# Kernel tuning notes

Hardware: AMD Instinct MI355X
Metric: run time of the kernel (lower is better)

## Reference

```python
import jax, jax.numpy as jnp
import numpy as np

N_NODES = 200000
N_EDGES = 6400000
IN_DIM = 15      # pfc_input_dim
POS_DIM = 4      # positional_dim
OUT_DIM = 2      # vtx_classes + 1


def setup_inputs() -> dict:
    key = jax.random.key(0)
    k1, k2, k3, k4, k5, k6, k7 = jax.random.split(key, 7)
    x_pfc = jax.random.normal(k1, (N_NODES, IN_DIM), dtype=jnp.float32)
    edge_index = jax.random.randint(k2, (2, N_EDGES), 0, N_NODES, dtype=jnp.int64)
    s_in = 1.0 / np.sqrt(IN_DIM)
    s_pos = 1.0 / np.sqrt(POS_DIM)
    # PointTransformerConv params: lin, lin_src, lin_dst (no bias), pos_nn = Linear(4, 2)
    W_lin = jax.random.uniform(k3, (OUT_DIM, IN_DIM), jnp.float32, -s_in, s_in)
    W_src = jax.random.uniform(k4, (OUT_DIM, IN_DIM), jnp.float32, -s_in, s_in)
    W_dst = jax.random.uniform(k5, (OUT_DIM, IN_DIM), jnp.float32, -s_in, s_in)
    W_pos = jax.random.uniform(k6, (OUT_DIM, POS_DIM), jnp.float32, -s_pos, s_pos)
    b_pos = jax.random.uniform(k7, (OUT_DIM,), jnp.float32, -s_pos, s_pos)
    return {"x_pfc": x_pfc, "edge_index": edge_index, "W_lin": W_lin,
            "W_src": W_src, "W_dst": W_dst, "W_pos": W_pos, "b_pos": b_pos}


def reference(x_pfc, edge_index, W_lin, W_src, W_dst, W_pos, b_pos):
    n = x_pfc.shape[0]
    pos = x_pfc[:, :POS_DIM]
    # original forward calls ptc_only(x, pos, edge_index.flip(0)):
    # source j = edge_index[1], target i = edge_index[0]
    j = edge_index[1]
    i = edge_index[0]
    # node-level linear maps (N x OUT_DIM)
    v = x_pfc @ W_lin.T
    a_src = x_pfc @ W_src.T
    a_dst = x_pfc @ W_dst.T
    # positional MLP on relative positions (E x OUT_DIM)
    delta = (pos[i] - pos[j]) @ W_pos.T + b_pos
    alpha = a_dst[i] - a_src[j] + delta
    # segment softmax over incoming edges of each target node i
    m = jax.ops.segment_max(alpha, i, num_segments=n)  # -inf for empty segments (never indexed)
    e = jnp.exp(alpha - m[i])
    denom = jax.ops.segment_sum(e, i, num_segments=n)
    attn = e / (denom[i] + 1e-16)
    msg = attn * (v[j] + delta)
    return jax.ops.segment_sum(msg, i, num_segments=n)
```

## Files before the change

### kernel.cpp

```cpp
#include <hip/hip_runtime.h>

#define N_NODES 200000
#define N_EDGES 6400000
#define IN_DIM 15
#define POS_DIM 4

#define CSHIFT 9
#define CMASK 511
#define CW 512
#define NCOARSE ((N_NODES + CW - 1) >> CSHIFT)
#define CHUNK 16384
#define NBLK ((N_EDGES + CHUNK - 1) / CHUNK)
#define CAP 17408
#define HCAP 8704

typedef unsigned uv4 __attribute__((ext_vector_type(4)));


__global__ void node_prep(const float* __restrict__ x,
                          const float* __restrict__ Wlin,
                          const float* __restrict__ Wsrc,
                          const float* __restrict__ Wpos,
                          float4* __restrict__ tabJ,
                          unsigned* __restrict__ gcnt)
{
    int n = blockIdx.x * blockDim.x + threadIdx.x;
    if (n < NCOARSE) gcnt[n] = 0u;
    if (n >= N_NODES) return;
    const float* xp = x + (long)n * IN_DIM;
    float xv[IN_DIM];
#pragma unroll
    for (int k = 0; k < IN_DIM; ++k) xv[k] = xp[k];

    float p0 = 0.f, p1 = 0.f;
#pragma unroll
    for (int k = 0; k < POS_DIM; ++k) {
        p0 += Wpos[k] * xv[k];
        p1 += Wpos[POS_DIM + k] * xv[k];
    }
    float v0 = 0.f, v1 = 0.f, as0 = 0.f, as1 = 0.f;
#pragma unroll
    for (int k = 0; k < IN_DIM; ++k) {
        float xk = xv[k];
        v0  += Wlin[k] * xk;  v1  += Wlin[IN_DIM + k] * xk;
        as0 += Wsrc[k] * xk;  as1 += Wsrc[IN_DIM + k] * xk;
    }
    tabJ[n] = make_float4(as0 + p0, as1 + p1, v0 - p0, v1 - p1);
}

__global__ void scatter_kernel(const int* __restrict__ idx,
                               unsigned* __restrict__ gcnt,
                               unsigned* __restrict__ packed)
{
    __shared__ unsigned stage[CHUNK];
    __shared__ unsigned cnt[512];
    __shared__ unsigned lloc[512];
    __shared__ unsigned gdst[NCOARSE];
    __shared__ unsigned wsum[8];
    int b = blockIdx.x;
    int t = threadIdx.x;
    int lane = t & 63, wid = t >> 6;
    long s0 = (long)b * CHUNK;
    int end = (int)min((long)CHUNK, (long)N_EDGES - s0);
    cnt[t] = 0u;
    __syncthreads();
    for (int e = t * 4; e < end; e += 2048) {
        int4 iv = *(const int4*)(idx + s0 + e);
        atomicAdd(&cnt[iv.x >> CSHIFT], 1u);
        atomicAdd(&cnt[iv.y >> CSHIFT], 1u);
        atomicAdd(&cnt[iv.z >> CSHIFT], 1u);
        atomicAdd(&cnt[iv.w >> CSHIFT], 1u);
    }
    __syncthreads();
    unsigned v = cnt[t];
    unsigned s = v;
#pragma unroll
    for (int off = 1; off < 64; off <<= 1) {
        unsigned u = __shfl_up(s, off, 64);
        if (lane >= off) s += u;
    }
    if (lane == 63) wsum[wid] = s;
    __syncthreads();
    unsigned woff = 0;
#pragma unroll
    for (int w = 0; w < 8; ++w) woff += (w < wid) ? wsum[w] : 0u;
    {
        unsigned ex = woff + s - v;
        lloc[t] = ex;
        cnt[t] = ex;
        if (t < NCOARSE) gdst[t] = atomicAdd(&gcnt[t], v);
    }
    __syncthreads();
    for (int e = t * 4; e < end; e += 2048) {
        int4 iv = *(const int4*)(idx + s0 + e);
        int4 jv = *(const int4*)(idx + N_EDGES + s0 + e);
        unsigned r0 = atomicAdd(&cnt[iv.x >> CSHIFT], 1u);
        unsigned r1 = atomicAdd(&cnt[iv.y >> CSHIFT], 1u);
        unsigned r2 = atomicAdd(&cnt[iv.z >> CSHIFT], 1u);
        unsigned r3 = atomicAdd(&cnt[iv.w >> CSHIFT], 1u);
        stage[r0] = ((unsigned)jv.x << CSHIFT) | (unsigned)(iv.x & CMASK);
        stage[r1] = ((unsigned)jv.y << CSHIFT) | (unsigned)(iv.y & CMASK);
        stage[r2] = ((unsigned)jv.z << CSHIFT) | (unsigned)(iv.z & CMASK);
        stage[r3] = ((unsigned)jv.w << CSHIFT) | (unsigned)(iv.w & CMASK);
    }
    __syncthreads();
    for (int bk = wid; bk < NCOARSE; bk += 8) {
        unsigned st  = lloc[bk];
        unsigned len = lloc[bk + 1] - st;
        unsigned gb  = gdst[bk];
        unsigned rem = (gb < (unsigned)CAP) ? (unsigned)CAP - gb : 0u;
        if (len > rem) len = rem;
        unsigned* dst = packed + (size_t)bk * CAP + gb;
        for (unsigned e = lane; e < len; e += 64u)
            dst[e] = stage[st + e];
    }
}

__global__ __launch_bounds__(256) void
bucket_agg_kernel(const unsigned* __restrict__ packed,
                  const unsigned* __restrict__ gcnt,
                  const float* __restrict__ x,
                  const float* __restrict__ Wdst,
                  const float* __restrict__ Wpos,
                  const float4* __restrict__ tabJ,
                  const float* __restrict__ bpos,
                  float2* __restrict__ out)
{
    __shared__ unsigned cache[HCAP + 512];
    __shared__ unsigned cnt[256], cur[256];
    __shared__ unsigned wsum[4];
    int blk = blockIdx.x;
    int k = blk >> 1;
    unsigned half = (unsigned)(blk & 1);
    int t = threadIdx.x;
    int lane = t & 63, wid = t >> 6;
    float b0 = bpos[0], b1 = bpos[1];
    int gn = (k << CSHIFT) + ((int)half << 8) + t;

    float p0 = 0.f, p1 = 0.f, ad0 = 0.f, ad1 = 0.f;
    if (gn < N_NODES) {
        const float* xp = x + (long)gn * IN_DIM;
        float xv[IN_DIM];
#pragma unroll
        for (int q = 0; q < IN_DIM; ++q) xv[q] = xp[q];
#pragma unroll
        for (int q = 0; q < POS_DIM; ++q) {
            p0 += Wpos[q] * xv[q];
            p1 += Wpos[POS_DIM + q] * xv[q];
        }
#pragma unroll
        for (int q = 0; q < IN_DIM; ++q) {
            ad0 += Wdst[q] * xv[q];
            ad1 += Wdst[IN_DIM + q] * xv[q];
        }
    }
    float a0 = ad0 + p0 + b0, a1 = ad1 + p1 + b1;
    float sn0 = 0.f, sn1 = 0.f, sd0 = 0.f, sd1 = 0.f;

    unsigned n = min(gcnt[k], (unsigned)CAP);
    const unsigned* pk = packed + (size_t)k * CAP;

#define KEEP(w) ((((w) & CMASK) >> 8) == half)
    cnt[t] = 0u;
    __syncthreads();
    for (unsigned e = 4u * t; e < n; e += 1024u) {
        uv4 p = *(const uv4*)(pk + e);
        if (KEEP(p.x))               atomicAdd(&cnt[p.x & 255u], 1u);
        if (e + 1 < n && KEEP(p.y))  atomicAdd(&cnt[p.y & 255u], 1u);
        if (e + 2 < n && KEEP(p.z))  atomicAdd(&cnt[p.z & 255u], 1u);
        if (e + 3 < n && KEEP(p.w))  atomicAdd(&cnt[p.w & 255u], 1u);
    }
    __syncthreads();
    unsigned v = cnt[t];
    unsigned s = v;
#pragma unroll
    for (int off = 1; off < 64; off <<= 1) {
        unsigned u = __shfl_up(s, off, 64);
        if (lane >= off) s += u;
    }
    if (lane == 63) wsum[wid] = s;
    __syncthreads();
    unsigned woff = 0;
#pragma unroll
    for (int w = 0; w < 4; ++w) woff += (w < wid) ? wsum[w] : 0u;
    unsigned deg = v;
    unsigned st  = woff + s - v + (unsigned)t;
    cur[t] = st;
    __syncthreads();
    for (unsigned e = 4u * t; e < n; e += 1024u) {
        uv4 p = __builtin_nontemporal_load((const uv4*)(pk + e));
        if (KEEP(p.x))              { unsigned pos = atomicAdd(&cur[p.x & 255u], 1u); cache[pos] = p.x >> CSHIFT; }
        if (e + 1 < n && KEEP(p.y)) { unsigned pos = atomicAdd(&cur[p.y & 255u], 1u); cache[pos] = p.y >> CSHIFT; }
        if (e + 2 < n && KEEP(p.z)) { unsigned pos = atomicAdd(&cur[p.z & 255u], 1u); cache[pos] = p.z >> CSHIFT; }
        if (e + 3 < n && KEEP(p.w)) { unsigned pos = atomicAdd(&cur[p.w & 255u], 1u); cache[pos] = p.w >> CSHIFT; }
    }
#undef KEEP
    __syncthreads();
    unsigned e = 0;
    for (; e + 8u <= deg; e += 8u) {
        unsigned j0 = cache[st + e],     j1 = cache[st + e + 1];
        unsigned j2 = cache[st + e + 2], j3 = cache[st + e + 3];
        unsigned j4 = cache[st + e + 4], j5 = cache[st + e + 5];
        unsigned j6 = cache[st + e + 6], j7 = cache[st + e + 7];
        float4 f0 = tabJ[j0], f1 = tabJ[j1], f2 = tabJ[j2], f3 = tabJ[j3];
        float4 f4 = tabJ[j4], f5 = tabJ[j5], f6 = tabJ[j6], f7 = tabJ[j7];
        float e00 = __expf(a0 - f0.x), e01 = __expf(a1 - f0.y);
        float e10 = __expf(a0 - f1.x), e11 = __expf(a1 - f1.y);
        float e20 = __expf(a0 - f2.x), e21 = __expf(a1 - f2.y);
        float e30 = __expf(a0 - f3.x), e31 = __expf(a1 - f3.y);
        float e40 = __expf(a0 - f4.x), e41 = __expf(a1 - f4.y);
        float e50 = __expf(a0 - f5.x), e51 = __expf(a1 - f5.y);
        float e60 = __expf(a0 - f6.x), e61 = __expf(a1 - f6.y);
        float e70 = __expf(a0 - f7.x), e71 = __expf(a1 - f7.y);
        sn0 += e00 * f0.z + e10 * f1.z + e20 * f2.z + e30 * f3.z
             + e40 * f4.z + e50 * f5.z + e60 * f6.z + e70 * f7.z;
        sn1 += e01 * f0.w + e11 * f1.w + e21 * f2.w + e31 * f3.w
             + e41 * f4.w + e51 * f5.w + e61 * f6.w + e71 * f7.w;
        sd0 += e00 + e10 + e20 + e30 + e40 + e50 + e60 + e70;
        sd1 += e01 + e11 + e21 + e31 + e41 + e51 + e61 + e71;
    }
    for (; e < deg; ++e) {
        unsigned j = cache[st + e];
        float4 fj = tabJ[j];
        float e0 = __expf(a0 - fj.x), e1 = __expf(a1 - fj.y);
        sn0 += e0 * fj.z;  sn1 += e1 * fj.w;
        sd0 += e0;         sd1 += e1;
    }

    if (gn >= N_NODES) return;
    float o0 = (sn0 + (p0 + b0) * sd0) / (sd0 + 1e-16f);
    float o1 = (sn1 + (p1 + b1) * sd1) / (sd1 + 1e-16f);
    out[gn] = make_float2(o0, o1);
}

extern "C" void kernel_launch(void* const* d_in, const int* in_sizes, int n_in,
                              void* d_out, int out_size, void* d_ws, size_t ws_size,
                              hipStream_t stream) {
    const float* x    = (const float*)d_in[0];
    const int*   idx  = (const int*)d_in[1];
    const float* Wlin = (const float*)d_in[2];
    const float* Wsrc = (const float*)d_in[3];
    const float* Wdst = (const float*)d_in[4];
    const float* Wpos = (const float*)d_in[5];
    const float* bpos = (const float*)d_in[6];
    float* out = (float*)d_out;

    char* ws = (char*)d_ws;
    size_t off = 0;
    float4* tabJ = (float4*)(ws + off); off += (size_t)N_NODES * 16;
    unsigned* packed = (unsigned*)(ws + off); off += (size_t)NCOARSE * CAP * 4;
    unsigned* gcnt   = (unsigned*)(ws + off); off += (size_t)NCOARSE * 4;

    node_prep<<<(N_NODES + 255) / 256, 256, 0, stream>>>(x, Wlin, Wsrc, Wpos,
                                                         tabJ, gcnt);
    scatter_kernel<<<NBLK, 512, 0, stream>>>(idx, gcnt, packed);
    bucket_agg_kernel<<<NCOARSE * 2, 256, 0, stream>>>(packed, gcnt,
                                                       x, Wdst, Wpos, tabJ, bpos,
                                                       (float2*)out);
}
```

Baseline: 172.6 us.

## Use 256-node buckets so aggregation reads only its own edges, split rows across two threads

Bucket width shrinks from 512 to 256 nodes. Each aggregation block now reads only its own bucket instead of two half-blocks each re-reading a shared 512-node bucket and filtering, which halves the packed-edge reads. The scatter kernel keeps the first-pass index loads in registers rather than reloading them, and handles 1024 buckets per block with two counters per thread. In aggregation, 512 threads work on 256 rows, with two threads splitting each row's neighbour list and combining via a lane shuffle. The cost is more buckets and global atomics in scatter, with smaller per-bucket capacity (CAP 9216) that could overflow on skewed inputs.

After: 204.8 us. 18.7% more time.

```diff
diff --git a/kernel.cpp b/kernel.cpp
--- a/kernel.cpp
+++ b/kernel.cpp
@@ -5,14 +5,12 @@
 #define IN_DIM 15
 #define POS_DIM 4
 
-#define CSHIFT 9
-#define CMASK 511
-#define CW 512
-#define NCOARSE ((N_NODES + CW - 1) >> CSHIFT)
-#define CHUNK 16384
+#define BSHIFT 8
+#define BMASK 255
+#define NB ((N_NODES + 255) >> 8)
+#define CHUNK 8192
 #define NBLK ((N_EDGES + CHUNK - 1) / CHUNK)
-#define CAP 17408
-#define HCAP 8704
+#define CAP 9216
 
 typedef unsigned uv4 __attribute__((ext_vector_type(4)));
 
@@ -25,7 +23,7 @@
                           unsigned* __restrict__ gcnt)
 {
     int n = blockIdx.x * blockDim.x + threadIdx.x;
-    if (n < NCOARSE) gcnt[n] = 0u;
+    if (n < NB) gcnt[n] = 0u;
     if (n >= N_NODES) return;
     const float* xp = x + (long)n * IN_DIM;
     float xv[IN_DIM];
@@ -48,32 +46,39 @@
     tabJ[n] = make_float4(as0 + p0, as1 + p1, v0 - p0, v1 - p1);
 }
 
-__global__ void scatter_kernel(const int* __restrict__ idx,
-                               unsigned* __restrict__ gcnt,
-                               unsigned* __restrict__ packed)
+__global__ __launch_bounds__(512) void
+scatter_kernel(const int* __restrict__ idx,
+               unsigned* __restrict__ gcnt,
+               unsigned* __restrict__ packed)
 {
     __shared__ unsigned stage[CHUNK];
-    __shared__ unsigned cnt[512];
-    __shared__ unsigned lloc[512];
-    __shared__ unsigned gdst[NCOARSE];
+    __shared__ unsigned cnt[1024];
+    __shared__ unsigned lloc[1024];
+    __shared__ unsigned gdst[NB];
     __shared__ unsigned wsum[8];
     int b = blockIdx.x;
     int t = threadIdx.x;
     int lane = t & 63, wid = t >> 6;
     long s0 = (long)b * CHUNK;
     int end = (int)min((long)CHUNK, (long)N_EDGES - s0);
-    cnt[t] = 0u;
-    __syncthreads();
-    for (int e = t * 4; e < end; e += 2048) {
-        int4 iv = *(const int4*)(idx + s0 + e);
-        atomicAdd(&cnt[iv.x >> CSHIFT], 1u);
-        atomicAdd(&cnt[iv.y >> CSHIFT], 1u);
-        atomicAdd(&cnt[iv.z >> CSHIFT], 1u);
-        atomicAdd(&cnt[iv.w >> CSHIFT], 1u);
-    }
-    __syncthreads();
-    unsigned v = cnt[t];
-    unsigned s = v;
+    cnt[t] = 0u; cnt[t + 512] = 0u;
+    __syncthreads();
+    int4 myi[4];
+    {
+        int rr = 0;
+        for (int e = t * 4; e < end; e += 2048, ++rr) {
+            int4 iv = *(const int4*)(idx + s0 + e);
+            myi[rr] = iv;
+            atomicAdd(&cnt[iv.x >> BSHIFT], 1u);
+            atomicAdd(&cnt[iv.y >> BSHIFT], 1u);
+            atomicAdd(&cnt[iv.z >> BSHIFT], 1u);
+            atomicAdd(&cnt[iv.w >> BSHIFT], 1u);
+        }
+    }
+    __syncthreads();
+    unsigned c0 = cnt[2 * t], c1 = cnt[2 * t + 1];
+    unsigned pv = c0 + c1;
+    unsigned s = pv;
 #pragma unroll
     for (int off = 1; off < 64; off <<= 1) {
         unsigned u = __shfl_up(s, off, 64);
@@ -81,30 +86,37 @@
     }
     if (lane == 63) wsum[wid] = s;
     __syncthreads();
-    unsigned woff = 0;
-#pragma unroll
-    for (int w = 0; w < 8; ++w) woff += (w < wid) ? wsum[w] : 0u;
     {
-        unsigned ex = woff + s - v;
-        lloc[t] = ex;
-        cnt[t] = ex;
-        if (t < NCOARSE) gdst[t] = atomicAdd(&gcnt[t], v);
-    }
-    __syncthreads();
-    for (int e = t * 4; e < end; e += 2048) {
-        int4 iv = *(const int4*)(idx + s0 + e);
-        int4 jv = *(const int4*)(idx + N_EDGES + s0 + e);
-        unsigned r0 = atomicAdd(&cnt[iv.x >> CSHIFT], 1u);
-        unsigned r1 = atomicAdd(&cnt[iv.y >> CSHIFT], 1u);
-        unsigned r2 = atomicAdd(&cnt[iv.z >> CSHIFT], 1u);
-        unsigned r3 = atomicAdd(&cnt[iv.w >> CSHIFT], 1u);
-        stage[r0] = ((unsigned)jv.x << CSHIFT) | (unsigned)(iv.x & CMASK);
-        stage[r1] = ((unsigned)jv.y << CSHIFT) | (unsigned)(iv.y & CMASK);
-        stage[r2] = ((unsigned)jv.z << CSHIFT) | (unsigned)(iv.z & CMASK);
-        stage[r3] = ((unsigned)jv.w << CSHIFT) | (unsigned)(iv.w & CMASK);
-    }
-    __syncthreads();
-    for (int bk = wid; bk < NCOARSE; bk += 8) {
+        unsigned woff = 0;
+#pragma unroll
+        for (int w = 0; w < 8; ++w) woff += (w < wid) ? wsum[w] : 0u;
+        unsigned exc = woff + s - pv;
+        lloc[2 * t] = exc;  lloc[2 * t + 1] = exc + c0;
+        cnt[2 * t]  = exc;  cnt[2 * t + 1]  = exc + c0;
+    }
+    __syncthreads();
+    for (int bk = t; bk < NB; bk += 512) {
+        unsigned len = lloc[bk + 1] - lloc[bk];
+        gdst[bk] = len ? atomicAdd(&gcnt[bk], len) : 0u;
+    }
+    __syncthreads();
+    {
+        int rr = 0;
+        for (int e = t * 4; e < end; e += 2048, ++rr) {
+            int4 iv = myi[rr];
+            int4 jv = *(const int4*)(idx + N_EDGES + s0 + e);
+            unsigned r0 = atomicAdd(&cnt[iv.x >> BSHIFT], 1u);
+            unsigned r1 = atomicAdd(&cnt[iv.y >> BSHIFT], 1u);
+            unsigned r2 = atomicAdd(&cnt[iv.z >> BSHIFT], 1u);
+            unsigned r3 = atomicAdd(&cnt[iv.w >> BSHIFT], 1u);
+            stage[r0] = ((unsigned)jv.x << BSHIFT) | ((unsigned)iv.x & BMASK);
+            stage[r1] = ((unsigned)jv.y << BSHIFT) | ((unsigned)iv.y & BMASK);
+            stage[r2] = ((unsigned)jv.z << BSHIFT) | ((unsigned)iv.z & BMASK);
+            stage[r3] = ((unsigned)jv.w << BSHIFT) | ((unsigned)iv.w & BMASK);
+        }
+    }
+    __syncthreads();
+    for (int bk = wid; bk < NB; bk += 8) {
         unsigned st  = lloc[bk];
         unsigned len = lloc[bk + 1] - st;
         unsigned gb  = gdst[bk];
@@ -116,7 +128,7 @@
     }
 }
 
-__global__ __launch_bounds__(256) void
+__global__ __launch_bounds__(512) void
 bucket_agg_kernel(const unsigned* __restrict__ packed,
                   const unsigned* __restrict__ gcnt,
                   const float* __restrict__ x,
@@ -126,16 +138,15 @@
                   const float* __restrict__ bpos,
                   float2* __restrict__ out)
 {
-    __shared__ unsigned cache[HCAP + 512];
+    __shared__ unsigned cache[CAP + 256];
     __shared__ unsigned cnt[256], cur[256];
     __shared__ unsigned wsum[4];
-    int blk = blockIdx.x;
-    int k = blk >> 1;
-    unsigned half = (unsigned)(blk & 1);
+    int k = blockIdx.x;
     int t = threadIdx.x;
     int lane = t & 63, wid = t >> 6;
+    int r = t >> 1, sub = t & 1;
     float b0 = bpos[0], b1 = bpos[1];
-    int gn = (k << CSHIFT) + ((int)half << 8) + t;
+    int gn = (k << BSHIFT) + r;
 
     float p0 = 0.f, p1 = 0.f, ad0 = 0.f, ad1 = 0.f;
     if (gn < N_NODES) {
@@ -157,51 +168,58 @@
     float a0 = ad0 + p0 + b0, a1 = ad1 + p1 + b1;
     float sn0 = 0.f, sn1 = 0.f, sd0 = 0.f, sd1 = 0.f;
 
+    if (t < 256) cnt[t] = 0u;
+    __syncthreads();
+
     unsigned n = min(gcnt[k], (unsigned)CAP);
     const unsigned* pk = packed + (size_t)k * CAP;
 
-#define KEEP(w) ((((w) & CMASK) >> 8) == half)
-    cnt[t] = 0u;
-    __syncthreads();
-    for (unsigned e = 4u * t; e < n; e += 1024u) {
+    for (unsigned e = 4u * t; e < n; e += 2048u) {
         uv4 p = *(const uv4*)(pk + e);
-        if (KEEP(p.x))               atomicAdd(&cnt[p.x & 255u], 1u);
-        if (e + 1 < n && KEEP(p.y))  atomicAdd(&cnt[p.y & 255u], 1u);
-        if (e + 2 < n && KEEP(p.z))  atomicAdd(&cnt[p.z & 255u], 1u);
-        if (e + 3 < n && KEEP(p.w))  atomicAdd(&cnt[p.w & 255u], 1u);
-    }
-    __syncthreads();
-    unsigned v = cnt[t];
-    unsigned s = v;
-#pragma unroll
-    for (int off = 1; off < 64; off <<= 1) {
-        unsigned u = __shfl_up(s, off, 64);
-        if (lane >= off) s += u;
-    }
-    if (lane == 63) wsum[wid] = s;
-    __syncthreads();
-    unsigned woff = 0;
-#pragma unroll
-    for (int w = 0; w < 4; ++w) woff += (w < wid) ? wsum[w] : 0u;
-    unsigned deg = v;
-    unsigned st  = woff + s - v + (unsigned)t;
-    cur[t] = st;
-    __syncthreads();
-    for (unsigned e = 4u * t; e < n; e += 1024u) {
+        atomicAdd(&cnt[p.x & BMASK], 1u);
+        if (e + 1 < n) atomicAdd(&cnt[p.y & BMASK], 1u);
+        if (e + 2 < n) atomicAdd(&cnt[p.z & BMASK], 1u);
+        if (e + 3 < n) atomicAdd(&cnt[p.w & BMASK], 1u);
+    }
+    __syncthreads();
+    unsigned v = 0, s = 0;
+    if (t < 256) {
+        v = cnt[t];
+        s = v;
+#pragma unroll
+        for (int off = 1; off < 64; off <<= 1) {
+            unsigned u = __shfl_up(s, off, 64);
+            if (lane >= off) s += u;
+        }
+        if (lane == 63) wsum[wid] = s;
+    }
+    __syncthreads();
+    if (t < 256) {
+        unsigned woff = 0;
+#pragma unroll
+        for (int w = 0; w < 4; ++w) woff += (w < wid) ? wsum[w] : 0u;
+        cur[t] = woff + s - v + (unsigned)t;
+    }
+    __syncthreads();
+    for (unsigned e = 4u * t; e < n; e += 2048u) {
         uv4 p = __builtin_nontemporal_load((const uv4*)(pk + e));
-        if (KEEP(p.x))              { unsigned pos = atomicAdd(&cur[p.x & 255u], 1u); cache[pos] = p.x >> CSHIFT; }
-        if (e + 1 < n && KEEP(p.y)) { unsigned pos = atomicAdd(&cur[p.y & 255u], 1u); cache[pos] = p.y >> CSHIFT; }
-        if (e + 2 < n && KEEP(p.z)) { unsigned pos = atomicAdd(&cur[p.z & 255u], 1u); cache[pos] = p.z >> CSHIFT; }
-        if (e + 3 < n && KEEP(p.w)) { unsigned pos = atomicAdd(&cur[p.w & 255u], 1u); cache[pos] = p.w >> CSHIFT; }
-    }
-#undef KEEP
-    __syncthreads();
+        { unsigned pos = atomicAdd(&cur[p.x & BMASK], 1u); cache[pos] = p.x >> BSHIFT; }
+        if (e + 1 < n) { unsigned pos = atomicAdd(&cur[p.y & BMASK], 1u); cache[pos] = p.y >> BSHIFT; }
+        if (e + 2 < n) { unsigned pos = atomicAdd(&cur[p.z & BMASK], 1u); cache[pos] = p.z >> BSHIFT; }
+        if (e + 3 < n) { unsigned pos = atomicAdd(&cur[p.w & BMASK], 1u); cache[pos] = p.w >> BSHIFT; }
+    }
+    __syncthreads();
+    unsigned deg   = cnt[r];
+    unsigned st    = cur[r] - deg;
+    unsigned half0 = (deg + 1) >> 1;
+    unsigned myst  = st + (sub ? half0 : 0u);
+    unsigned mylen = sub ? (deg - half0) : half0;
     unsigned e = 0;
-    for (; e + 8u <= deg; e += 8u) {
-        unsigned j0 = cache[st + e],     j1 = cache[st + e + 1];
-        unsigned j2 = cache[st + e + 2], j3 = cache[st + e + 3];
-        unsigned j4 = cache[st + e + 4], j5 = cache[st + e + 5];
-        unsigned j6 = cache[st + e + 6], j7 = cache[st + e + 7];
+    for (; e + 8u <= mylen; e += 8u) {
+        unsigned j0 = cache[myst + e],     j1 = cache[myst + e + 1];
+        unsigned j2 = cache[myst + e + 2], j3 = cache[myst + e + 3];
+        unsigned j4 = cache[myst + e + 4], j5 = cache[myst + e + 5];
+        unsigned j6 = cache[myst + e + 6], j7 = cache[myst + e + 7];
         float4 f0 = tabJ[j0], f1 = tabJ[j1], f2 = tabJ[j2], f3 = tabJ[j3];
         float4 f4 = tabJ[j4], f5 = tabJ[j5], f6 = tabJ[j6], f7 = tabJ[j7];
         float e00 = __expf(a0 - f0.x), e01 = __expf(a1 - f0.y);
@@ -219,15 +237,17 @@
         sd0 += e00 + e10 + e20 + e30 + e40 + e50 + e60 + e70;
         sd1 += e01 + e11 + e21 + e31 + e41 + e51 + e61 + e71;
     }
-    for (; e < deg; ++e) {
-        unsigned j = cache[st + e];
+    for (; e < mylen; ++e) {
+        unsigned j = cache[myst + e];
         float4 fj = tabJ[j];
         float e0 = __expf(a0 - fj.x), e1 = __expf(a1 - fj.y);
         sn0 += e0 * fj.z;  sn1 += e1 * fj.w;
         sd0 += e0;         sd1 += e1;
     }
-
-    if (gn >= N_NODES) return;
+    sn0 += __shfl_xor(sn0, 1);  sn1 += __shfl_xor(sn1, 1);
+    sd0 += __shfl_xor(sd0, 1);  sd1 += __shfl_xor(sd1, 1);
+
+    if (sub != 0 || gn >= N_NODES) return;
     float o0 = (sn0 + (p0 + b0) * sd0) / (sd0 + 1e-16f);
     float o1 = (sn1 + (p1 + b1) * sd1) / (sd1 + 1e-16f);
     out[gn] = make_float2(o0, o1);
@@ -248,13 +268,13 @@
     char* ws = (char*)d_ws;
     size_t off = 0;
     float4* tabJ = (float4*)(ws + off); off += (size_t)N_NODES * 16;
-    unsigned* packed = (unsigned*)(ws + off); off += (size_t)NCOARSE * CAP * 4;
-    unsigned* gcnt   = (unsigned*)(ws + off); off += (size_t)NCOARSE * 4;
+    unsigned* packed = (unsigned*)(ws + off); off += (size_t)NB * CAP * 4;
+    unsigned* gcnt   = (unsigned*)(ws + off); off += (size_t)NB * 4;
 
     node_prep<<<(N_NODES + 255) / 256, 256, 0, stream>>>(x, Wlin, Wsrc, Wpos,
                                                          tabJ, gcnt);
     scatter_kernel<<<NBLK, 512, 0, stream>>>(idx, gcnt, packed);
-    bucket_agg_kernel<<<NCOARSE * 2, 256, 0, stream>>>(packed, gcnt,
-                                                       x, Wdst, Wpos, tabJ, bpos,
-                                                       (float2*)out);
-}
+    bucket_agg_kernel<<<NB, 512, 0, stream>>>(packed, gcnt,
+                                              x, Wdst, Wpos, tabJ, bpos,
+                                              (float2*)out);
+}
```

## Process whole coarse bucket per 1024-thread block with two threads per node

Applied to the files above, without the earlier changes.

The aggregation kernel now handles a full 512-node bucket in one 1024-thread block instead of two half-bucket blocks. Each block reads its packed edge list once rather than twice, and each node's edges are split across two threads whose partial sums are combined with a shuffle. The scatter kernel also keeps the target indices from its counting pass in registers, so it does not reload them, and it uses nontemporal loads. The trade-off is fewer, larger blocks with more shared memory each, which may lower occupancy, and there are only about 391 blocks to spread across the device.

Result: no change. 170.0 us (-1.5%).

```diff
diff --git a/kernel.cpp b/kernel.cpp
--- a/kernel.cpp
+++ b/kernel.cpp
@@ -7,14 +7,13 @@
 
 #define CSHIFT 9
 #define CMASK 511
-#define CW 512
-#define NCOARSE ((N_NODES + CW - 1) >> CSHIFT)
+#define NCOARSE ((N_NODES + 511) >> 9)
 #define CHUNK 16384
 #define NBLK ((N_EDGES + CHUNK - 1) / CHUNK)
 #define CAP 17408
-#define HCAP 8704
 
 typedef unsigned uv4 __attribute__((ext_vector_type(4)));
+typedef int      iv4 __attribute__((ext_vector_type(4)));
 
 
 __global__ void node_prep(const float* __restrict__ x,
@@ -48,9 +47,10 @@
     tabJ[n] = make_float4(as0 + p0, as1 + p1, v0 - p0, v1 - p1);
 }
 
-__global__ void scatter_kernel(const int* __restrict__ idx,
-                               unsigned* __restrict__ gcnt,
-                               unsigned* __restrict__ packed)
+__global__ __launch_bounds__(512) void
+scatter_kernel(const int* __restrict__ idx,
+               unsigned* __restrict__ gcnt,
+               unsigned* __restrict__ packed)
 {
     __shared__ unsigned stage[CHUNK];
     __shared__ unsigned cnt[512];
@@ -64,12 +64,17 @@
     int end = (int)min((long)CHUNK, (long)N_EDGES - s0);
     cnt[t] = 0u;
     __syncthreads();
-    for (int e = t * 4; e < end; e += 2048) {
-        int4 iv = *(const int4*)(idx + s0 + e);
-        atomicAdd(&cnt[iv.x >> CSHIFT], 1u);
-        atomicAdd(&cnt[iv.y >> CSHIFT], 1u);
-        atomicAdd(&cnt[iv.z >> CSHIFT], 1u);
-        atomicAdd(&cnt[iv.w >> CSHIFT], 1u);
+    iv4 myi[8];
+    {
+        int rr = 0;
+        for (int e = t * 4; e < end; e += 2048, ++rr) {
+            iv4 iv = __builtin_nontemporal_load((const iv4*)(idx + s0 + e));
+            myi[rr] = iv;
+            atomicAdd(&cnt[iv.x >> CSHIFT], 1u);
+            atomicAdd(&cnt[iv.y >> CSHIFT], 1u);
+            atomicAdd(&cnt[iv.z >> CSHIFT], 1u);
+            atomicAdd(&cnt[iv.w >> CSHIFT], 1u);
+        }
     }
     __syncthreads();
     unsigned v = cnt[t];
@@ -91,22 +96,25 @@
         if (t < NCOARSE) gdst[t] = atomicAdd(&gcnt[t], v);
     }
     __syncthreads();
-    for (int e = t * 4; e < end; e += 2048) {
-        int4 iv = *(const int4*)(idx + s0 + e);
-        int4 jv = *(const int4*)(idx + N_EDGES + s0 + e);
-        unsigned r0 = atomicAdd(&cnt[iv.x >> CSHIFT], 1u);
-        unsigned r1 = atomicAdd(&cnt[iv.y >> CSHIFT], 1u);
-        unsigned r2 = atomicAdd(&cnt[iv.z >> CSHIFT], 1u);
-        unsigned r3 = atomicAdd(&cnt[iv.w >> CSHIFT], 1u);
-        stage[r0] = ((unsigned)jv.x << CSHIFT) | (unsigned)(iv.x & CMASK);
-        stage[r1] = ((unsigned)jv.y << CSHIFT) | (unsigned)(iv.y & CMASK);
-        stage[r2] = ((unsigned)jv.z << CSHIFT) | (unsigned)(iv.z & CMASK);
-        stage[r3] = ((unsigned)jv.w << CSHIFT) | (unsigned)(iv.w & CMASK);
+    {
+        int rr = 0;
+        for (int e = t * 4; e < end; e += 2048, ++rr) {
+            iv4 iv = myi[rr];
+            iv4 jv = __builtin_nontemporal_load((const iv4*)(idx + N_EDGES + s0 + e));
+            unsigned r0 = atomicAdd(&cnt[iv.x >> CSHIFT], 1u);
+            unsigned r1 = atomicAdd(&cnt[iv.y >> CSHIFT], 1u);
+            unsigned r2 = atomicAdd(&cnt[iv.z >> CSHIFT], 1u);
+            unsigned r3 = atomicAdd(&cnt[iv.w >> CSHIFT], 1u);
+            stage[r0] = ((unsigned)jv.x << CSHIFT) | ((unsigned)iv.x & CMASK);
+            stage[r1] = ((unsigned)jv.y << CSHIFT) | ((unsigned)iv.y & CMASK);
+            stage[r2] = ((unsigned)jv.z << CSHIFT) | ((unsigned)iv.z & CMASK);
+            stage[r3] = ((unsigned)jv.w << CSHIFT) | ((unsigned)iv.w & CMASK);
+        }
     }
     __syncthreads();
     for (int bk = wid; bk < NCOARSE; bk += 8) {
         unsigned st  = lloc[bk];
-        unsigned len = lloc[bk + 1] - st;
+        unsigned len = ((bk + 1 < 512) ? lloc[bk + 1] : (unsigned)end) - st;
         unsigned gb  = gdst[bk];
         unsigned rem = (gb < (unsigned)CAP) ? (unsigned)CAP - gb : 0u;
         if (len > rem) len = rem;
@@ -116,7 +124,7 @@
     }
 }
 
-__global__ __launch_bounds__(256) void
+__global__ __launch_bounds__(1024) void
 bucket_agg_kernel(const unsigned* __restrict__ packed,
                   const unsigned* __restrict__ gcnt,
                   const float* __restrict__ x,
@@ -126,16 +134,15 @@
                   const float* __restrict__ bpos,
                   float2* __restrict__ out)
 {
-    __shared__ unsigned cache[HCAP + 512];
-    __shared__ unsigned cnt[256], cur[256];
-    __shared__ unsigned wsum[4];
-    int blk = blockIdx.x;
-    int k = blk >> 1;
-    unsigned half = (unsigned)(blk & 1);
+    __shared__ unsigned cache[CAP + 512];
+    __shared__ unsigned cnt[512], cur[512];
+    __shared__ unsigned wsum[8];
+    int k = blockIdx.x;
     int t = threadIdx.x;
-    int lane = t & 63, wid = t >> 6;
+    int lane = t & 63;
+    int r = t >> 1, sub = t & 1;
     float b0 = bpos[0], b1 = bpos[1];
-    int gn = (k << CSHIFT) + ((int)half << 8) + t;
+    int gn = (k << CSHIFT) + r;
 
     float p0 = 0.f, p1 = 0.f, ad0 = 0.f, ad1 = 0.f;
     if (gn < N_NODES) {
@@ -157,51 +164,59 @@
     float a0 = ad0 + p0 + b0, a1 = ad1 + p1 + b1;
     float sn0 = 0.f, sn1 = 0.f, sd0 = 0.f, sd1 = 0.f;
 
+    if (t < 512) cnt[t] = 0u;
+    __syncthreads();
+
     unsigned n = min(gcnt[k], (unsigned)CAP);
     const unsigned* pk = packed + (size_t)k * CAP;
 
-#define KEEP(w) ((((w) & CMASK) >> 8) == half)
-    cnt[t] = 0u;
-    __syncthreads();
-    for (unsigned e = 4u * t; e < n; e += 1024u) {
+    for (unsigned e = 4u * t; e < n; e += 4096u) {
         uv4 p = *(const uv4*)(pk + e);
-        if (KEEP(p.x))               atomicAdd(&cnt[p.x & 255u], 1u);
-        if (e + 1 < n && KEEP(p.y))  atomicAdd(&cnt[p.y & 255u], 1u);
-        if (e + 2 < n && KEEP(p.z))  atomicAdd(&cnt[p.z & 255u], 1u);
-        if (e + 3 < n && KEEP(p.w))  atomicAdd(&cnt[p.w & 255u], 1u);
-    }
-    __syncthreads();
-    unsigned v = cnt[t];
-    unsigned s = v;
-#pragma unroll
-    for (int off = 1; off < 64; off <<= 1) {
-        unsigned u = __shfl_up(s, off, 64);
-        if (lane >= off) s += u;
-    }
-    if (lane == 63) wsum[wid] = s;
-    __syncthreads();
-    unsigned woff = 0;
-#pragma unroll
-    for (int w = 0; w < 4; ++w) woff += (w < wid) ? wsum[w] : 0u;
-    unsigned deg = v;
-    unsigned st  = woff + s - v + (unsigned)t;
-    cur[t] = st;
-    __syncthreads();
-    for (unsigned e = 4u * t; e < n; e += 1024u) {
+        atomicAdd(&cnt[p.x & CMASK], 1u);
+        if (e + 1 < n) atomicAdd(&cnt[p.y & CMASK], 1u);
+        if (e + 2 < n) atomicAdd(&cnt[p.z & CMASK], 1u);
+        if (e + 3 < n) atomicAdd(&cnt[p.w & CMASK], 1u);
+    }
+    __syncthreads();
+    unsigned v = 0, s = 0;
+    if (t < 512) {
+        v = cnt[t];
+        s = v;
+#pragma unroll
+        for (int off = 1; off < 64; off <<= 1) {
+            unsigned u = __shfl_up(s, off, 64);
+            if (lane >= off) s += u;
+        }
+        if (lane == 63) wsum[t >> 6] = s;
+    }
+    __syncthreads();
+    if (t < 512) {
+        int wid = t >> 6;
+        unsigned woff = 0;
+#pragma unroll
+        for (int w = 0; w < 8; ++w) woff += (w < wid) ? wsum[w] : 0u;
+        cur[t] = woff + s - v + (unsigned)t;
+    }
+    __syncthreads();
+    for (unsigned e = 4u * t; e < n; e += 4096u) {
         uv4 p = __builtin_nontemporal_load((const uv4*)(pk + e));
-        if (KEEP(p.x))              { unsigned pos = atomicAdd(&cur[p.x & 255u], 1u); cache[pos] = p.x >> CSHIFT; }
-        if (e + 1 < n && KEEP(p.y)) { unsigned pos = atomicAdd(&cur[p.y & 255u], 1u); cache[pos] = p.y >> CSHIFT; }
-        if (e + 2 < n && KEEP(p.z)) { unsigned pos = atomicAdd(&cur[p.z & 255u], 1u); cache[pos] = p.z >> CSHIFT; }
-        if (e + 3 < n && KEEP(p.w)) { unsigned pos = atomicAdd(&cur[p.w & 255u], 1u); cache[pos] = p.w >> CSHIFT; }
-    }
-#undef KEEP
-    __syncthreads();
+        { unsigned pos = atomicAdd(&cur[p.x & CMASK], 1u); cache[pos] = p.x >> CSHIFT; }
+        if (e + 1 < n) { unsigned pos = atomicAdd(&cur[p.y & CMASK], 1u); cache[pos] = p.y >> CSHIFT; }
+        if (e + 2 < n) { unsigned pos = atomicAdd(&cur[p.z & CMASK], 1u); cache[pos] = p.z >> CSHIFT; }
+        if (e + 3 < n) { unsigned pos = atomicAdd(&cur[p.w & CMASK], 1u); cache[pos] = p.w >> CSHIFT; }
+    }
+    __syncthreads();
+    unsigned deg   = cnt[r];
+    unsigned st    = cur[r] - deg;
+    unsigned half0 = (deg + 1) >> 1;
+    unsigned myst  = st + (sub ? half0 : 0u);
+    unsigned mylen = sub ? (deg - half0) : half0;
     unsigned e = 0;
-    for (; e + 8u <= deg; e += 8u) {
-        unsigned j0 = cache[st + e],     j1 = cache[st + e + 1];
-        unsigned j2 = cache[st + e + 2], j3 = cache[st + e + 3];
-        unsigned j4 = cache[st + e + 4], j5 = cache[st + e + 5];
-        unsigned j6 = cache[st + e + 6], j7 = cache[st + e + 7];
+    for (; e + 8u <= mylen; e += 8u) {
+        unsigned j0 = cache[myst + e],     j1 = cache[myst + e + 1];
+        unsigned j2 = cache[myst + e + 2], j3 = cache[myst + e + 3];
+        unsigned j4 = cache[myst + e + 4], j5 = cache[myst + e + 5];
+        unsigned j6 = cache[myst + e + 6], j7 = cache[myst + e + 7];
         float4 f0 = tabJ[j0], f1 = tabJ[j1], f2 = tabJ[j2], f3 = tabJ[j3];
         float4 f4 = tabJ[j4], f5 = tabJ[j5], f6 = tabJ[j6], f7 = tabJ[j7];
         float e00 = __expf(a0 - f0.x), e01 = __expf(a1 - f0.y);
@@ -219,15 +234,17 @@
         sd0 += e00 + e10 + e20 + e30 + e40 + e50 + e60 + e70;
         sd1 += e01 + e11 + e21 + e31 + e41 + e51 + e61 + e71;
     }
-    for (; e < deg; ++e) {
-        unsigned j = cache[st + e];
+    for (; e < mylen; ++e) {
+        unsigned j = cache[myst + e];
         float4 fj = tabJ[j];
         float e0 = __expf(a0 - fj.x), e1 = __expf(a1 - fj.y);
         sn0 += e0 * fj.z;  sn1 += e1 * fj.w;
         sd0 += e0;         sd1 += e1;
     }
-
-    if (gn >= N_NODES) return;
+    sn0 += __shfl_xor(sn0, 1);  sn1 += __shfl_xor(sn1, 1);
+    sd0 += __shfl_xor(sd0, 1);  sd1 += __shfl_xor(sd1, 1);
+
+    if (sub != 0 || gn >= N_NODES) return;
     float o0 = (sn0 + (p0 + b0) * sd0) / (sd0 + 1e-16f);
     float o1 = (sn1 + (p1 + b1) * sd1) / (sd1 + 1e-16f);
     out[gn] = make_float2(o0, o1);
@@ -254,7 +271,7 @@
     node_prep<<<(N_NODES + 255) / 256, 256, 0, stream>>>(x, Wlin, Wsrc, Wpos,
                                                          tabJ, gcnt);
     scatter_kernel<<<NBLK, 512, 0, stream>>>(idx, gcnt, packed);
-    bucket_agg_kernel<<<NCOARSE * 2, 256, 0, stream>>>(packed, gcnt,
-                                                       x, Wdst, Wpos, tabJ, bpos,
-                                                       (float2*)out);
-}
+    bucket_agg_kernel<<<NCOARSE, 1024, 0, stream>>>(packed, gcnt,
+                                                    x, Wdst, Wpos, tabJ, bpos,
+                                                    (float2*)out);
+}
```
